# Performance work log

Measured on AMD Instinct MI355X. Metric: run time of the kernel, lower is better.

## Reference

```python
import jax, jax.numpy as jnp
import numpy as np

NUM_CLASSES = 81
NMS_THRESHOLD = 0.4
MAX_BOXES = 300
NEG = -1e9  # score used to mark suppressed / background boxes


def setup_inputs() -> dict:
    key = jax.random.key(0)
    k1, k2, k3, k4, k5 = jax.random.split(key, 5)
    N = 300000
    # realistic boxes: centers in [0,800), sizes in [1,101)
    cx = jax.random.uniform(k1, (N,), jnp.float32) * 800.0
    cy = jax.random.uniform(k2, (N,), jnp.float32) * 800.0
    w = jax.random.uniform(k3, (N,), jnp.float32) * 100.0 + 1.0
    h = jax.random.uniform(k4, (N,), jnp.float32) * 100.0 + 1.0
    boxes = jnp.stack([cx - w / 2, cy - h / 2, cx + w / 2, cy + h / 2], axis=-1)
    boxes = boxes[None]  # [1, N, 4]
    classification = jax.random.normal(k5, (1, N, NUM_CLASSES), jnp.float32)
    return {"boxes": boxes, "classification": classification}


def _nms_select(boxes, scores, max_boxes, iou_threshold):
    # boxes: [N,4] (x1,y1,x2,y2); scores: [N]. Greedy NMS, fixed max_boxes iterations.
    x1, y1, x2, y2 = boxes[:, 0], boxes[:, 1], boxes[:, 2], boxes[:, 3]
    areas = jnp.maximum(x2 - x1, 0.0) * jnp.maximum(y2 - y1, 0.0)

    def body(scores_c, _):
        idx = jnp.argmax(scores_c)
        valid = scores_c[idx] > NEG / 2
        b = boxes[idx]
        xx1 = jnp.maximum(b[0], x1)
        yy1 = jnp.maximum(b[1], y1)
        xx2 = jnp.minimum(b[2], x2)
        yy2 = jnp.minimum(b[3], y2)
        inter = jnp.maximum(xx2 - xx1, 0.0) * jnp.maximum(yy2 - yy1, 0.0)
        union = areas[idx] + areas - inter
        iou = inter / jnp.maximum(union, 1e-8)
        # suppress everything overlapping the selected box (includes itself, iou=1)
        new_scores = jnp.where(iou > iou_threshold, NEG, scores_c)
        return new_scores, (idx, valid)

    _, (idxs, valids) = jax.lax.scan(body, scores, None, length=max_boxes)
    return idxs, valids


def reference(boxes, classification):
    b = boxes.reshape(-1, 4)                      # [N,4]
    cls = classification.reshape(-1, NUM_CLASSES)  # [N,C]
    scores = jnp.max(cls, axis=1)                  # [N]
    labels = jnp.argmax(cls, axis=1)               # [N]
    # filter background (label==0) by masking scores instead of dynamic gather
    scores = jnp.where(labels > 0, scores, NEG)
    idxs, valid = _nms_select(b, scores, MAX_BOXES, NMS_THRESHOLD)
    v = valid[:, None].astype(b.dtype)
    out_boxes = b[idxs] * v                        # [max_boxes,4], zero-padded
    out_cls = cls[idxs] * v                        # [max_boxes,C], zero-padded
    return out_boxes[None], out_cls[None]
```

## Files before the change

kernel.cpp:

```cpp
#include <hip/hip_runtime.h>
#include <stdint.h>

#define NUM_CLASSES 81
#define MAX_BOXES 300
#define NEG_SCORE (-1000000000.0f)
#define IOU_THR 0.4f
#define MMAX 2048
#define MWORDS (MMAX / 64)

static constexpr size_t OFF_SCORES = 0;
static constexpr size_t OFF_CAREA  = 0x1F0000;
static constexpr size_t OFF_COARSE = 0x200000;
static constexpr size_t OFF_FINE   = 0x201000;
static constexpr size_t OFF_CTRL   = 0x202000;
static constexpr size_t OFF_RANK   = 0x203000;
static constexpr size_t OFF_KEYS   = 0x208000;
static constexpr size_t OFF_CIDX   = 0x210000;
static constexpr size_t OFF_CBOX   = 0x214000;
static constexpr size_t OFF_ACC    = 0x224000;
static constexpr size_t OFF_MATRIX = 0x228000;

__device__ __forceinline__ uint32_t float_ordered(float f) {
    uint32_t b = __float_as_uint(f);
    return (b & 0x80000000u) ? ~b : (b | 0x80000000u);
}

__device__ __forceinline__ uint64_t readlane_u64(uint64_t v, int srclane) {
    uint32_t lo = (uint32_t)__builtin_amdgcn_readlane((int)(uint32_t)v, srclane);
    uint32_t hi = (uint32_t)__builtin_amdgcn_readlane((int)(uint32_t)(v >> 32), srclane);
    return ((uint64_t)hi << 32) | lo;
}

__global__ void score_kernel(const float* __restrict__ cls, float* __restrict__ scores,
                             uint32_t* __restrict__ coarse, uint32_t* __restrict__ fine,
                             uint32_t* __restrict__ ctrl, uint32_t* __restrict__ rank, int n) {
    if (blockIdx.x == 0) {
        int t = threadIdx.x;
        if (t < 256) { coarse[t] = 0; fine[t] = 0; }
        if (t < 8) ctrl[t] = 0;
        for (int r = t; r < MMAX; r += 256) rank[r] = 0;
    }
    const int q = threadIdx.x & 15;
    const int box = blockIdx.x * 16 + (threadIdx.x >> 4);
    const int cbox = box < n ? box : n - 1;
    const float* row = cls + (size_t)cbox * NUM_CLASSES;

    float v[5];
    #pragma unroll
    for (int it = 0; it < 5; ++it) v[it] = row[it * 16 + q];
    float e80 = row[80];

    float m = v[0];
    #pragma unroll
    for (int it = 1; it < 5; ++it) m = fmaxf(m, v[it]);
    m = (q == 15) ? fmaxf(m, e80) : m;
    m = fmaxf(m, __shfl_xor(m, 1));
    m = fmaxf(m, __shfl_xor(m, 2));
    m = fmaxf(m, __shfl_xor(m, 4));
    m = fmaxf(m, __shfl_xor(m, 8));

    if (q == 0 && box < n) {
        scores[box] = (v[0] == m) ? NEG_SCORE : m;
    }
}

__global__ void coarse_hist_kernel(const float* __restrict__ scores, uint32_t* __restrict__ coarse, int n) {
    __shared__ uint32_t h[256];
    for (int t = threadIdx.x; t < 256; t += blockDim.x) h[t] = 0;
    __syncthreads();
    for (int i = blockIdx.x * blockDim.x + threadIdx.x; i < n; i += gridDim.x * blockDim.x) {
        uint32_t o = float_ordered(scores[i]);
        atomicAdd(&h[o >> 24], 1u);
    }
    __syncthreads();
    for (int t = threadIdx.x; t < 256; t += blockDim.x)
        if (h[t]) atomicAdd(&coarse[t], h[t]);
}

__device__ __forceinline__ int select_coarse(const uint32_t* coarse, uint32_t* above_out) {
    uint32_t s = 0;
    for (int c = 255; c >= 0; --c) {
        uint32_t sc = s + coarse[c];
        if (sc > MMAX) { *above_out = s; return c; }
        s = sc;
    }
    *above_out = s;
    return -1;
}

__global__ void fine_hist_kernel(const float* __restrict__ scores, const uint32_t* __restrict__ coarse,
                                 uint32_t* __restrict__ fine, int n) {
    __shared__ int sC;
    __shared__ uint32_t h[256];
    if (threadIdx.x == 0) {
        uint32_t above;
        sC = select_coarse(coarse, &above);
    }
    for (int t = threadIdx.x; t < 256; t += blockDim.x) h[t] = 0;
    __syncthreads();
    int C = sC;
    if (C < 0) return;
    for (int i = blockIdx.x * blockDim.x + threadIdx.x; i < n; i += gridDim.x * blockDim.x) {
        uint32_t o = float_ordered(scores[i]);
        if ((int)(o >> 24) == C) atomicAdd(&h[(o >> 16) & 255u], 1u);
    }
    __syncthreads();
    for (int t = threadIdx.x; t < 256; t += blockDim.x)
        if (h[t]) atomicAdd(&fine[t], h[t]);
}

__global__ void compact_kernel(const float* __restrict__ scores, const uint32_t* __restrict__ coarse,
                               const uint32_t* __restrict__ fine, uint32_t* __restrict__ ctrl,
                               uint64_t* __restrict__ keys, int n) {
    __shared__ uint32_t sThr;
    if (threadIdx.x == 0) {
        uint32_t above;
        int C = select_coarse(coarse, &above);
        uint32_t thr;
        if (C < 0) {
            thr = 0;
        } else {
            uint32_t R = MMAX - above;
            uint32_t g = 0, F = 0;
            for (int f = 255; f >= 0; --f) {
                uint32_t gf = g + fine[f];
                if (gf > R) { F = (uint32_t)f + 1u; break; }
                g = gf;
            }
            thr = ((uint32_t)C << 8) | F;
        }
        sThr = thr;
    }
    __syncthreads();
    uint32_t thr = sThr;
    for (int i = blockIdx.x * blockDim.x + threadIdx.x; i < n; i += gridDim.x * blockDim.x) {
        uint32_t o = float_ordered(scores[i]);
        if ((o >> 16) >= thr) {
            uint32_t pos = atomicAdd(&ctrl[0], 1u);
            if (pos < MMAX)
                keys[pos] = ((uint64_t)o << 32) | (uint32_t)(~(uint32_t)i);
        }
    }
}

__global__ void rank_partial_kernel(const uint64_t* __restrict__ keys, const uint32_t* __restrict__ ctrl,
                                    uint32_t* __restrict__ rank) {
    __shared__ uint64_t kk[256];
    int M = (int)ctrl[0]; if (M > MMAX) M = MMAX;
    int cbase = blockIdx.x * 256;
    int jbase = blockIdx.y * 256;
    if (cbase >= M || jbase >= M) return;
    int t = threadIdx.x;
    int j = jbase + t;
    kk[t] = (j < M) ? keys[j] : 0ull;
    __syncthreads();
    int c = cbase + t;
    if (c >= M) return;
    uint64_t k = keys[c];
    int cnt = 0;
    #pragma unroll 8
    for (int u = 0; u < 256; ++u) cnt += (kk[u] > k) ? 1 : 0;
    if (cnt) atomicAdd(&rank[c], (uint32_t)cnt);
}

__global__ void scatter_kernel(const uint64_t* __restrict__ keys, const uint32_t* __restrict__ rank,
                               const uint32_t* __restrict__ ctrl, const float* __restrict__ boxes,
                               int* __restrict__ csorted_idx, float4* __restrict__ csorted_box,
                               float* __restrict__ careas) {
    int M = (int)ctrl[0]; if (M > MMAX) M = MMAX;
    int c = blockIdx.x * blockDim.x + threadIdx.x;
    if (c >= M) return;
    uint64_t k = keys[c];
    uint32_t r = rank[c];
    uint32_t idx = ~(uint32_t)k;
    float4 b = *(const float4*)(boxes + (size_t)idx * 4);
    csorted_idx[r] = (int)idx;
    csorted_box[r] = b;
    careas[r] = fmaxf(b.z - b.x, 0.f) * fmaxf(b.w - b.y, 0.f);
}

__global__ void matrix_kernel(const float4* __restrict__ cbox, const float* __restrict__ careas,
                              const uint32_t* __restrict__ ctrl, uint64_t* __restrict__ matrix) {
    int i = blockIdx.x;
    int M = (int)ctrl[0]; if (M > MMAX) M = MMAX;
    if (i >= M) return;
    int lane = threadIdx.x & 63;
    int wave = threadIdx.x >> 6;
    float4 bi = cbox[i];
    float ai = careas[i];
    int w0 = i >> 6;
    for (int w = w0 + wave; w < MWORDS; w += 4) {
        int j = (w << 6) | lane;
        bool sup = false;
        if (j < M) {
            float4 bj = cbox[j];
            float xx1 = fmaxf(bi.x, bj.x);
            float yy1 = fmaxf(bi.y, bj.y);
            float xx2 = fminf(bi.z, bj.z);
            float yy2 = fminf(bi.w, bj.w);
            float inter = fmaxf(xx2 - xx1, 0.f) * fmaxf(yy2 - yy1, 0.f);
            float uni = ai + careas[j] - inter;
            float iou = inter / fmaxf(uni, 1e-8f);
            sup = iou > IOU_THR;
        }
        uint64_t word = __ballot(sup ? 1 : 0);
        if (lane == 0) matrix[(size_t)i * MWORDS + w] = word;
    }
}

typedef const uint32_t __attribute__((address_space(1)))* glb_u32p;
typedef uint32_t __attribute__((address_space(3)))* lds_u32p;

__global__ void scan_kernel(const uint64_t* __restrict__ matrix, uint32_t* __restrict__ ctrl,
                            int* __restrict__ accepted) {
    __shared__ uint64_t sbuf[2][64][MWORDS];
    const int lane = threadIdx.x;
    const int l31 = lane & 31;
    int M = (int)ctrl[0]; if (M > MMAX) M = MMAX;
    uint64_t removed = 0;
    uint64_t wrd = 0;
    int acc = 0;

#define STAGE(BI, BASE)                                                          \
    {                                                                            \
        _Pragma("unroll")                                                        \
        for (int r_ = 0; r_ < 64; ++r_) {                                        \
            const uint32_t* gsrc =                                               \
                (const uint32_t*)(matrix + (size_t)((BASE) + r_) * MWORDS) + lane; \
            __builtin_amdgcn_global_load_lds((glb_u32p)gsrc,                     \
                                             (lds_u32p)&sbuf[BI][r_][0], 4, 0, 0); \
        }                                                                        \
    }

#define PROCESS(BI, BASE)                                                        \
    {                                                                            \
        uint64_t W[16];                                                          \
        _Pragma("unroll")                                                        \
        for (int w_ = 0; w_ < 16; ++w_) W[w_] = sbuf[BI][w_][l31];               \
        _Pragma("unroll")                                                        \
        for (int r_ = 0; r_ < 64; ++r_) {                                        \
            int i_ = (BASE) + r_;                                                \
            uint64_t row = W[r_ & 15];                                           \
            if (r_ + 16 < 64) W[r_ & 15] = sbuf[BI][r_ + 16][l31];               \
            if (r_ == 0) wrd = readlane_u64(removed, i_ >> 6);                   \
            if (i_ < M && acc < MAX_BOXES && !((wrd >> (i_ & 63)) & 1ull)) {     \
                if (lane == 0) accepted[acc] = i_;                               \
                removed |= row;                                                  \
                wrd = readlane_u64(removed, i_ >> 6);                            \
                ++acc;                                                           \
            }                                                                    \
        }                                                                        \
    }

    int nblocks = (M + 63) >> 6;
    if (nblocks > 0) {
        STAGE(0, 0);
        asm volatile("s_waitcnt vmcnt(0)" ::: "memory");
        int bi = 0;
        for (int b = 0; b < nblocks && acc < MAX_BOXES; ++b) {
            if (b + 1 < nblocks) STAGE(bi ^ 1, (b + 1) << 6);
            PROCESS(bi, b << 6);
            asm volatile("s_waitcnt vmcnt(0)" ::: "memory");
            bi ^= 1;
        }
    }
#undef STAGE
#undef PROCESS
    if (lane == 0) ctrl[1] = (uint32_t)acc;
}

__global__ void output_kernel(const float* __restrict__ boxes, const float* __restrict__ cls,
                              const int* __restrict__ csorted_idx, const int* __restrict__ accepted,
                              const uint32_t* __restrict__ ctrl, float* __restrict__ out, int total) {
    int e = blockIdx.x * blockDim.x + threadIdx.x;
    if (e >= total) return;
    int acc = (int)ctrl[1];
    float val = 0.0f;
    if (e < MAX_BOXES * 4) {
        int s = e >> 2, f = e & 3;
        if (s < acc) {
            int orig = csorted_idx[accepted[s]];
            val = boxes[(size_t)orig * 4 + f];
        }
    } else {
        int e2 = e - MAX_BOXES * 4;
        int s = e2 / NUM_CLASSES;
        int c = e2 - s * NUM_CLASSES;
        if (s < acc) {
            int orig = csorted_idx[accepted[s]];
            val = cls[(size_t)orig * NUM_CLASSES + c];
        }
    }
    out[e] = val;
}

extern "C" void kernel_launch(void* const* d_in, const int* in_sizes, int n_in,
                              void* d_out, int out_size, void* d_ws, size_t ws_size,
                              hipStream_t stream) {
    const float* boxes = (const float*)d_in[0];
    const float* cls   = (const float*)d_in[1];
    float* out = (float*)d_out;
    const int N = in_sizes[0] / 4;

    char* ws = (char*)d_ws;
    float*     scores      = (float*)(ws + OFF_SCORES);
    float*     careas      = (float*)(ws + OFF_CAREA);
    uint32_t*  coarse      = (uint32_t*)(ws + OFF_COARSE);
    uint32_t*  fine        = (uint32_t*)(ws + OFF_FINE);
    uint32_t*  ctrl        = (uint32_t*)(ws + OFF_CTRL);
    uint32_t*  rank        = (uint32_t*)(ws + OFF_RANK);
    uint64_t*  keys        = (uint64_t*)(ws + OFF_KEYS);
    int*       csorted_idx = (int*)(ws + OFF_CIDX);
    float4*    csorted_box = (float4*)(ws + OFF_CBOX);
    int*       accepted    = (int*)(ws + OFF_ACC);
    uint64_t*  matrix      = (uint64_t*)(ws + OFF_MATRIX);

    score_kernel<<<(N + 15) / 16, 256, 0, stream>>>(cls, scores, coarse, fine, ctrl, rank, N);
    coarse_hist_kernel<<<256, 256, 0, stream>>>(scores, coarse, N);
    fine_hist_kernel<<<256, 256, 0, stream>>>(scores, coarse, fine, N);
    compact_kernel<<<512, 256, 0, stream>>>(scores, coarse, fine, ctrl, keys, N);
    rank_partial_kernel<<<dim3(MMAX / 256, MMAX / 256), 256, 0, stream>>>(keys, ctrl, rank);
    scatter_kernel<<<MMAX / 256, 256, 0, stream>>>(keys, rank, ctrl, boxes, csorted_idx,
                                                   csorted_box, careas);
    matrix_kernel<<<MMAX, 256, 0, stream>>>(csorted_box, careas, ctrl, matrix);
    scan_kernel<<<1, 64, 0, stream>>>(matrix, ctrl, accepted);
    output_kernel<<<(out_size + 255) / 256, 256, 0, stream>>>(boxes, cls, csorted_idx, accepted,
                                                              ctrl, out, out_size);
}
```

Before: 109.0 us.

## Fuse all NMS stages into one cooperative persistent kernel with grid syncs

Replaces the nine separate kernel launches with a single cooperative kernel of 256 blocks that runs every stage in turn, separated by grid.sync(). The rank and scatter steps are merged: each of 8 blocks loads all keys into LDS and computes full ranks directly, so the rank buffer and its atomics go away. The aim is to remove per-launch overhead and inter-kernel gaps. In exchange, grid-wide barriers are paid at every stage, occupancy is limited to 256 blocks (the score pass over 300k rows now loops), and the large shared-memory union may reduce how many blocks fit per CU.

```diff
diff --git a/kernel.cpp b/kernel.cpp
--- a/kernel.cpp
+++ b/kernel.cpp
@@ -1,5 +1,8 @@
 #include <hip/hip_runtime.h>
+#include <hip/hip_cooperative_groups.h>
 #include <stdint.h>
+
+namespace cg = cooperative_groups;
 
 #define NUM_CLASSES 81
 #define MAX_BOXES 300
@@ -7,13 +10,14 @@
 #define IOU_THR 0.4f
 #define MMAX 2048
 #define MWORDS (MMAX / 64)
+#define GRID_BLOCKS 256
+#define BLOCK_THREADS 256
 
 static constexpr size_t OFF_SCORES = 0;
 static constexpr size_t OFF_CAREA  = 0x1F0000;
 static constexpr size_t OFF_COARSE = 0x200000;
 static constexpr size_t OFF_FINE   = 0x201000;
 static constexpr size_t OFF_CTRL   = 0x202000;
-static constexpr size_t OFF_RANK   = 0x203000;
 static constexpr size_t OFF_KEYS   = 0x208000;
 static constexpr size_t OFF_CIDX   = 0x210000;
 static constexpr size_t OFF_CBOX   = 0x214000;
@@ -29,52 +33,6 @@
     uint32_t lo = (uint32_t)__builtin_amdgcn_readlane((int)(uint32_t)v, srclane);
     uint32_t hi = (uint32_t)__builtin_amdgcn_readlane((int)(uint32_t)(v >> 32), srclane);
     return ((uint64_t)hi << 32) | lo;
-}
-
-__global__ void score_kernel(const float* __restrict__ cls, float* __restrict__ scores,
-                             uint32_t* __restrict__ coarse, uint32_t* __restrict__ fine,
-                             uint32_t* __restrict__ ctrl, uint32_t* __restrict__ rank, int n) {
-    if (blockIdx.x == 0) {
-        int t = threadIdx.x;
-        if (t < 256) { coarse[t] = 0; fine[t] = 0; }
-        if (t < 8) ctrl[t] = 0;
-        for (int r = t; r < MMAX; r += 256) rank[r] = 0;
-    }
-    const int q = threadIdx.x & 15;
-    const int box = blockIdx.x * 16 + (threadIdx.x >> 4);
-    const int cbox = box < n ? box : n - 1;
-    const float* row = cls + (size_t)cbox * NUM_CLASSES;
-
-    float v[5];
-    #pragma unroll
-    for (int it = 0; it < 5; ++it) v[it] = row[it * 16 + q];
-    float e80 = row[80];
-
-    float m = v[0];
-    #pragma unroll
-    for (int it = 1; it < 5; ++it) m = fmaxf(m, v[it]);
-    m = (q == 15) ? fmaxf(m, e80) : m;
-    m = fmaxf(m, __shfl_xor(m, 1));
-    m = fmaxf(m, __shfl_xor(m, 2));
-    m = fmaxf(m, __shfl_xor(m, 4));
-    m = fmaxf(m, __shfl_xor(m, 8));
-
-    if (q == 0 && box < n) {
-        scores[box] = (v[0] == m) ? NEG_SCORE : m;
-    }
-}
-
-__global__ void coarse_hist_kernel(const float* __restrict__ scores, uint32_t* __restrict__ coarse, int n) {
-    __shared__ uint32_t h[256];
-    for (int t = threadIdx.x; t < 256; t += blockDim.x) h[t] = 0;
-    __syncthreads();
-    for (int i = blockIdx.x * blockDim.x + threadIdx.x; i < n; i += gridDim.x * blockDim.x) {
-        uint32_t o = float_ordered(scores[i]);
-        atomicAdd(&h[o >> 24], 1u);
-    }
-    __syncthreads();
-    for (int t = threadIdx.x; t < 256; t += blockDim.x)
-        if (h[t]) atomicAdd(&coarse[t], h[t]);
 }
 
 __device__ __forceinline__ int select_coarse(const uint32_t* coarse, uint32_t* above_out) {
@@ -88,32 +46,95 @@
     return -1;
 }
 
-__global__ void fine_hist_kernel(const float* __restrict__ scores, const uint32_t* __restrict__ coarse,
-                                 uint32_t* __restrict__ fine, int n) {
+typedef const uint32_t __attribute__((address_space(1)))* glb_u32p;
+typedef uint32_t __attribute__((address_space(3)))* lds_u32p;
+
+union SmemU {
+    uint32_t h[256];
+    uint64_t kk[MMAX];
+    uint64_t sbuf[2][64][MWORDS];
+};
+
+__global__ void __launch_bounds__(BLOCK_THREADS) nms_mega(
+    const float* __restrict__ boxes, const float* __restrict__ cls,
+    float* __restrict__ out, char* __restrict__ ws, int n, int out_total) {
+    cg::grid_group grid = cg::this_grid();
+
+    float*     scores      = (float*)(ws + OFF_SCORES);
+    float*     careas      = (float*)(ws + OFF_CAREA);
+    uint32_t*  coarse      = (uint32_t*)(ws + OFF_COARSE);
+    uint32_t*  fine        = (uint32_t*)(ws + OFF_FINE);
+    uint32_t*  ctrl        = (uint32_t*)(ws + OFF_CTRL);
+    uint64_t*  keys        = (uint64_t*)(ws + OFF_KEYS);
+    int*       csorted_idx = (int*)(ws + OFF_CIDX);
+    float4*    csorted_box = (float4*)(ws + OFF_CBOX);
+    int*       accepted    = (int*)(ws + OFF_ACC);
+    uint64_t*  matrix      = (uint64_t*)(ws + OFF_MATRIX);
+
+    __shared__ SmemU sm;
     __shared__ int sC;
-    __shared__ uint32_t h[256];
-    if (threadIdx.x == 0) {
-        uint32_t above;
-        sC = select_coarse(coarse, &above);
-    }
-    for (int t = threadIdx.x; t < 256; t += blockDim.x) h[t] = 0;
-    __syncthreads();
-    int C = sC;
-    if (C < 0) return;
-    for (int i = blockIdx.x * blockDim.x + threadIdx.x; i < n; i += gridDim.x * blockDim.x) {
-        uint32_t o = float_ordered(scores[i]);
-        if ((int)(o >> 24) == C) atomicAdd(&h[(o >> 16) & 255u], 1u);
-    }
-    __syncthreads();
-    for (int t = threadIdx.x; t < 256; t += blockDim.x)
-        if (h[t]) atomicAdd(&fine[t], h[t]);
-}
-
-__global__ void compact_kernel(const float* __restrict__ scores, const uint32_t* __restrict__ coarse,
-                               const uint32_t* __restrict__ fine, uint32_t* __restrict__ ctrl,
-                               uint64_t* __restrict__ keys, int n) {
     __shared__ uint32_t sThr;
-    if (threadIdx.x == 0) {
+
+    const int tid = threadIdx.x;
+    const int bid = blockIdx.x;
+    const int nb  = gridDim.x;
+
+    if (bid == 0) {
+        if (tid < 256) { coarse[tid] = 0; fine[tid] = 0; }
+        if (tid < 8) ctrl[tid] = 0;
+    }
+    {
+        const int q = tid & 15;
+        const int g = tid >> 4;
+        for (int b0 = bid * 16; b0 < n; b0 += nb * 16) {
+            int box = b0 + g;
+            int cbox = box < n ? box : n - 1;
+            const float* row = cls + (size_t)cbox * NUM_CLASSES;
+            float v[5];
+            #pragma unroll
+            for (int it = 0; it < 5; ++it) v[it] = row[it * 16 + q];
+            float e80 = row[80];
+            float m = v[0];
+            #pragma unroll
+            for (int it = 1; it < 5; ++it) m = fmaxf(m, v[it]);
+            m = (q == 15) ? fmaxf(m, e80) : m;
+            m = fmaxf(m, __shfl_xor(m, 1));
+            m = fmaxf(m, __shfl_xor(m, 2));
+            m = fmaxf(m, __shfl_xor(m, 4));
+            m = fmaxf(m, __shfl_xor(m, 8));
+            if (q == 0 && box < n)
+                scores[box] = (v[0] == m) ? NEG_SCORE : m;
+        }
+    }
+    grid.sync();
+
+    for (int t = tid; t < 256; t += BLOCK_THREADS) sm.h[t] = 0;
+    __syncthreads();
+    for (int i = bid * BLOCK_THREADS + tid; i < n; i += nb * BLOCK_THREADS)
+        atomicAdd(&sm.h[float_ordered(scores[i]) >> 24], 1u);
+    __syncthreads();
+    for (int t = tid; t < 256; t += BLOCK_THREADS)
+        if (sm.h[t]) atomicAdd(&coarse[t], sm.h[t]);
+    grid.sync();
+
+    if (tid == 0) { uint32_t ab; sC = select_coarse(coarse, &ab); }
+    for (int t = tid; t < 256; t += BLOCK_THREADS) sm.h[t] = 0;
+    __syncthreads();
+    {
+        int C = sC;
+        if (C >= 0) {
+            for (int i = bid * BLOCK_THREADS + tid; i < n; i += nb * BLOCK_THREADS) {
+                uint32_t o = float_ordered(scores[i]);
+                if ((int)(o >> 24) == C) atomicAdd(&sm.h[(o >> 16) & 255u], 1u);
+            }
+        }
+    }
+    __syncthreads();
+    for (int t = tid; t < 256; t += BLOCK_THREADS)
+        if (sm.h[t]) atomicAdd(&fine[t], sm.h[t]);
+    grid.sync();
+
+    if (tid == 0) {
         uint32_t above;
         int C = select_coarse(coarse, &above);
         uint32_t thr;
@@ -132,166 +153,147 @@
         sThr = thr;
     }
     __syncthreads();
-    uint32_t thr = sThr;
-    for (int i = blockIdx.x * blockDim.x + threadIdx.x; i < n; i += gridDim.x * blockDim.x) {
-        uint32_t o = float_ordered(scores[i]);
-        if ((o >> 16) >= thr) {
-            uint32_t pos = atomicAdd(&ctrl[0], 1u);
-            if (pos < MMAX)
-                keys[pos] = ((uint64_t)o << 32) | (uint32_t)(~(uint32_t)i);
-        }
-    }
-}
-
-__global__ void rank_partial_kernel(const uint64_t* __restrict__ keys, const uint32_t* __restrict__ ctrl,
-                                    uint32_t* __restrict__ rank) {
-    __shared__ uint64_t kk[256];
+    {
+        uint32_t thr = sThr;
+        for (int i = bid * BLOCK_THREADS + tid; i < n; i += nb * BLOCK_THREADS) {
+            uint32_t o = float_ordered(scores[i]);
+            if ((o >> 16) >= thr) {
+                uint32_t pos = atomicAdd(&ctrl[0], 1u);
+                if (pos < MMAX)
+                    keys[pos] = ((uint64_t)o << 32) | (uint32_t)(~(uint32_t)i);
+            }
+        }
+    }
+    grid.sync();
+
     int M = (int)ctrl[0]; if (M > MMAX) M = MMAX;
-    int cbase = blockIdx.x * 256;
-    int jbase = blockIdx.y * 256;
-    if (cbase >= M || jbase >= M) return;
-    int t = threadIdx.x;
-    int j = jbase + t;
-    kk[t] = (j < M) ? keys[j] : 0ull;
-    __syncthreads();
-    int c = cbase + t;
-    if (c >= M) return;
-    uint64_t k = keys[c];
-    int cnt = 0;
-    #pragma unroll 8
-    for (int u = 0; u < 256; ++u) cnt += (kk[u] > k) ? 1 : 0;
-    if (cnt) atomicAdd(&rank[c], (uint32_t)cnt);
-}
-
-__global__ void scatter_kernel(const uint64_t* __restrict__ keys, const uint32_t* __restrict__ rank,
-                               const uint32_t* __restrict__ ctrl, const float* __restrict__ boxes,
-                               int* __restrict__ csorted_idx, float4* __restrict__ csorted_box,
-                               float* __restrict__ careas) {
-    int M = (int)ctrl[0]; if (M > MMAX) M = MMAX;
-    int c = blockIdx.x * blockDim.x + threadIdx.x;
-    if (c >= M) return;
-    uint64_t k = keys[c];
-    uint32_t r = rank[c];
-    uint32_t idx = ~(uint32_t)k;
-    float4 b = *(const float4*)(boxes + (size_t)idx * 4);
-    csorted_idx[r] = (int)idx;
-    csorted_box[r] = b;
-    careas[r] = fmaxf(b.z - b.x, 0.f) * fmaxf(b.w - b.y, 0.f);
-}
-
-__global__ void matrix_kernel(const float4* __restrict__ cbox, const float* __restrict__ careas,
-                              const uint32_t* __restrict__ ctrl, uint64_t* __restrict__ matrix) {
-    int i = blockIdx.x;
-    int M = (int)ctrl[0]; if (M > MMAX) M = MMAX;
-    if (i >= M) return;
-    int lane = threadIdx.x & 63;
-    int wave = threadIdx.x >> 6;
-    float4 bi = cbox[i];
-    float ai = careas[i];
-    int w0 = i >> 6;
-    for (int w = w0 + wave; w < MWORDS; w += 4) {
-        int j = (w << 6) | lane;
-        bool sup = false;
-        if (j < M) {
-            float4 bj = cbox[j];
-            float xx1 = fmaxf(bi.x, bj.x);
-            float yy1 = fmaxf(bi.y, bj.y);
-            float xx2 = fminf(bi.z, bj.z);
-            float yy2 = fminf(bi.w, bj.w);
-            float inter = fmaxf(xx2 - xx1, 0.f) * fmaxf(yy2 - yy1, 0.f);
-            float uni = ai + careas[j] - inter;
-            float iou = inter / fmaxf(uni, 1e-8f);
-            sup = iou > IOU_THR;
-        }
-        uint64_t word = __ballot(sup ? 1 : 0);
-        if (lane == 0) matrix[(size_t)i * MWORDS + w] = word;
-    }
-}
-
-typedef const uint32_t __attribute__((address_space(1)))* glb_u32p;
-typedef uint32_t __attribute__((address_space(3)))* lds_u32p;
-
-__global__ void scan_kernel(const uint64_t* __restrict__ matrix, uint32_t* __restrict__ ctrl,
-                            int* __restrict__ accepted) {
-    __shared__ uint64_t sbuf[2][64][MWORDS];
-    const int lane = threadIdx.x;
-    const int l31 = lane & 31;
-    int M = (int)ctrl[0]; if (M > MMAX) M = MMAX;
-    uint64_t removed = 0;
-    uint64_t wrd = 0;
-    int acc = 0;
-
-#define STAGE(BI, BASE)                                                          \
-    {                                                                            \
-        _Pragma("unroll")                                                        \
-        for (int r_ = 0; r_ < 64; ++r_) {                                        \
-            const uint32_t* gsrc =                                               \
+
+    if (bid < MMAX / BLOCK_THREADS) {
+        for (int i = tid; i < MMAX; i += BLOCK_THREADS)
+            sm.kk[i] = (i < M) ? keys[i] : 0ull;
+        __syncthreads();
+        int c = bid * BLOCK_THREADS + tid;
+        if (c < M) {
+            uint64_t k = sm.kk[c];
+            int cnt = 0;
+            #pragma unroll 8
+            for (int u = 0; u < MMAX; ++u) cnt += (sm.kk[u] > k) ? 1 : 0;
+            uint32_t idx = ~(uint32_t)k;
+            float4 b = *(const float4*)(boxes + (size_t)idx * 4);
+            csorted_idx[cnt] = (int)idx;
+            csorted_box[cnt] = b;
+            careas[cnt] = fmaxf(b.z - b.x, 0.f) * fmaxf(b.w - b.y, 0.f);
+        }
+        __syncthreads();
+    }
+    grid.sync();
+
+    {
+        int lane = tid & 63;
+        int wave = tid >> 6;
+        for (int i = bid; i < M; i += nb) {
+            float4 bi = csorted_box[i];
+            float ai = careas[i];
+            int w0 = i >> 6;
+            for (int w = w0 + wave; w < MWORDS; w += 4) {
+                int j = (w << 6) | lane;
+                bool sup = false;
+                if (j < M) {
+                    float4 bj = csorted_box[j];
+                    float xx1 = fmaxf(bi.x, bj.x);
+                    float yy1 = fmaxf(bi.y, bj.y);
+                    float xx2 = fminf(bi.z, bj.z);
+                    float yy2 = fminf(bi.w, bj.w);
+                    float inter = fmaxf(xx2 - xx1, 0.f) * fmaxf(yy2 - yy1, 0.f);
+                    float uni = ai + careas[j] - inter;
+                    float iou = inter / fmaxf(uni, 1e-8f);
+                    sup = iou > IOU_THR;
+                }
+                uint64_t word = __ballot(sup ? 1 : 0);
+                if (lane == 0) matrix[(size_t)i * MWORDS + w] = word;
+            }
+        }
+    }
+    grid.sync();
+
+    if (bid == 0 && tid < 64) {
+        const int lane = tid;
+        const int l31 = lane & 31;
+        uint64_t removed = 0;
+        uint64_t wrd = 0;
+        int acc = 0;
+
+#define STAGE(BI, BASE)                                                            \
+    {                                                                              \
+        _Pragma("unroll")                                                          \
+        for (int r_ = 0; r_ < 64; ++r_) {                                          \
+            const uint32_t* gsrc =                                                 \
                 (const uint32_t*)(matrix + (size_t)((BASE) + r_) * MWORDS) + lane; \
-            __builtin_amdgcn_global_load_lds((glb_u32p)gsrc,                     \
-                                             (lds_u32p)&sbuf[BI][r_][0], 4, 0, 0); \
-        }                                                                        \
-    }
-
-#define PROCESS(BI, BASE)                                                        \
-    {                                                                            \
-        uint64_t W[16];                                                          \
-        _Pragma("unroll")                                                        \
-        for (int w_ = 0; w_ < 16; ++w_) W[w_] = sbuf[BI][w_][l31];               \
-        _Pragma("unroll")                                                        \
-        for (int r_ = 0; r_ < 64; ++r_) {                                        \
-            int i_ = (BASE) + r_;                                                \
-            uint64_t row = W[r_ & 15];                                           \
-            if (r_ + 16 < 64) W[r_ & 15] = sbuf[BI][r_ + 16][l31];               \
-            if (r_ == 0) wrd = readlane_u64(removed, i_ >> 6);                   \
-            if (i_ < M && acc < MAX_BOXES && !((wrd >> (i_ & 63)) & 1ull)) {     \
-                if (lane == 0) accepted[acc] = i_;                               \
-                removed |= row;                                                  \
-                wrd = readlane_u64(removed, i_ >> 6);                            \
-                ++acc;                                                           \
-            }                                                                    \
-        }                                                                        \
-    }
-
-    int nblocks = (M + 63) >> 6;
-    if (nblocks > 0) {
-        STAGE(0, 0);
-        asm volatile("s_waitcnt vmcnt(0)" ::: "memory");
-        int bi = 0;
-        for (int b = 0; b < nblocks && acc < MAX_BOXES; ++b) {
-            if (b + 1 < nblocks) STAGE(bi ^ 1, (b + 1) << 6);
-            PROCESS(bi, b << 6);
+            __builtin_amdgcn_global_load_lds((glb_u32p)gsrc,                       \
+                                             (lds_u32p)&sm.sbuf[BI][r_][0], 4, 0, 0); \
+        }                                                                          \
+    }
+
+#define PROCESS(BI, BASE)                                                          \
+    {                                                                              \
+        uint64_t W[16];                                                            \
+        _Pragma("unroll")                                                          \
+        for (int w_ = 0; w_ < 16; ++w_) W[w_] = sm.sbuf[BI][w_][l31];              \
+        _Pragma("unroll")                                                          \
+        for (int r_ = 0; r_ < 64; ++r_) {                                          \
+            int i_ = (BASE) + r_;                                                  \
+            uint64_t row = W[r_ & 15];                                             \
+            if (r_ + 16 < 64) W[r_ & 15] = sm.sbuf[BI][r_ + 16][l31];              \
+            if (r_ == 0) wrd = readlane_u64(removed, i_ >> 6);                     \
+            if (i_ < M && acc < MAX_BOXES && !((wrd >> (i_ & 63)) & 1ull)) {       \
+                if (lane == 0) accepted[acc] = i_;                                 \
+                removed |= row;                                                    \
+                wrd = readlane_u64(removed, i_ >> 6);                              \
+                ++acc;                                                             \
+            }                                                                      \
+        }                                                                          \
+    }
+
+        int nblocks = (M + 63) >> 6;
+        if (nblocks > 0) {
+            STAGE(0, 0);
             asm volatile("s_waitcnt vmcnt(0)" ::: "memory");
-            bi ^= 1;
-        }
-    }
+            int bi = 0;
+            for (int b = 0; b < nblocks && acc < MAX_BOXES; ++b) {
+                if (b + 1 < nblocks) STAGE(bi ^ 1, (b + 1) << 6);
+                PROCESS(bi, b << 6);
+                asm volatile("s_waitcnt vmcnt(0)" ::: "memory");
+                bi ^= 1;
+            }
+        }
 #undef STAGE
 #undef PROCESS
-    if (lane == 0) ctrl[1] = (uint32_t)acc;
-}
-
-__global__ void output_kernel(const float* __restrict__ boxes, const float* __restrict__ cls,
-                              const int* __restrict__ csorted_idx, const int* __restrict__ accepted,
-                              const uint32_t* __restrict__ ctrl, float* __restrict__ out, int total) {
-    int e = blockIdx.x * blockDim.x + threadIdx.x;
-    if (e >= total) return;
-    int acc = (int)ctrl[1];
-    float val = 0.0f;
-    if (e < MAX_BOXES * 4) {
-        int s = e >> 2, f = e & 3;
-        if (s < acc) {
-            int orig = csorted_idx[accepted[s]];
-            val = boxes[(size_t)orig * 4 + f];
-        }
-    } else {
-        int e2 = e - MAX_BOXES * 4;
-        int s = e2 / NUM_CLASSES;
-        int c = e2 - s * NUM_CLASSES;
-        if (s < acc) {
-            int orig = csorted_idx[accepted[s]];
-            val = cls[(size_t)orig * NUM_CLASSES + c];
-        }
-    }
-    out[e] = val;
+        if (lane == 0) ctrl[1] = (uint32_t)acc;
+    }
+    grid.sync();
+
+    {
+        int acc = (int)ctrl[1];
+        for (int e = bid * BLOCK_THREADS + tid; e < out_total; e += nb * BLOCK_THREADS) {
+            float val = 0.0f;
+            if (e < MAX_BOXES * 4) {
+                int s = e >> 2, f = e & 3;
+                if (s < acc) {
+                    int orig = csorted_idx[accepted[s]];
+                    val = boxes[(size_t)orig * 4 + f];
+                }
+            } else {
+                int e2 = e - MAX_BOXES * 4;
+                int s = e2 / NUM_CLASSES;
+                int c = e2 - s * NUM_CLASSES;
+                if (s < acc) {
+                    int orig = csorted_idx[accepted[s]];
+                    val = cls[(size_t)orig * NUM_CLASSES + c];
+                }
+            }
+            out[e] = val;
+        }
+    }
 }
 
 extern "C" void kernel_launch(void* const* d_in, const int* in_sizes, int n_in,
@@ -300,30 +302,12 @@
     const float* boxes = (const float*)d_in[0];
     const float* cls   = (const float*)d_in[1];
     float* out = (float*)d_out;
-    const int N = in_sizes[0] / 4;
-
     char* ws = (char*)d_ws;
-    float*     scores      = (float*)(ws + OFF_SCORES);
-    float*     careas      = (float*)(ws + OFF_CAREA);
-    uint32_t*  coarse      = (uint32_t*)(ws + OFF_COARSE);
-    uint32_t*  fine        = (uint32_t*)(ws + OFF_FINE);
-    uint32_t*  ctrl        = (uint32_t*)(ws + OFF_CTRL);
-    uint32_t*  rank        = (uint32_t*)(ws + OFF_RANK);
-    uint64_t*  keys        = (uint64_t*)(ws + OFF_KEYS);
-    int*       csorted_idx = (int*)(ws + OFF_CIDX);
-    float4*    csorted_box = (float4*)(ws + OFF_CBOX);
-    int*       accepted    = (int*)(ws + OFF_ACC);
-    uint64_t*  matrix      = (uint64_t*)(ws + OFF_MATRIX);
-
-    score_kernel<<<(N + 15) / 16, 256, 0, stream>>>(cls, scores, coarse, fine, ctrl, rank, N);
-    coarse_hist_kernel<<<256, 256, 0, stream>>>(scores, coarse, N);
-    fine_hist_kernel<<<256, 256, 0, stream>>>(scores, coarse, fine, N);
-    compact_kernel<<<512, 256, 0, stream>>>(scores, coarse, fine, ctrl, keys, N);
-    rank_partial_kernel<<<dim3(MMAX / 256, MMAX / 256), 256, 0, stream>>>(keys, ctrl, rank);
-    scatter_kernel<<<MMAX / 256, 256, 0, stream>>>(keys, rank, ctrl, boxes, csorted_idx,
-                                                   csorted_box, careas);
-    matrix_kernel<<<MMAX, 256, 0, stream>>>(csorted_box, careas, ctrl, matrix);
-    scan_kernel<<<1, 64, 0, stream>>>(matrix, ctrl, accepted);
-    output_kernel<<<(out_size + 255) / 256, 256, 0, stream>>>(boxes, cls, csorted_idx, accepted,
-                                                              ctrl, out, out_size);
-}
+    int N = in_sizes[0] / 4;
+    int out_total = out_size;
+
+    void* args[] = {(void*)&boxes, (void*)&cls, (void*)&out, (void*)&ws,
+                    (void*)&N, (void*)&out_total};
+    hipLaunchCooperativeKernel((const void*)nms_mega, dim3(GRID_BLOCKS),
+                               dim3(BLOCK_THREADS), args, 0, stream);
+}
```

Measured after the change: 345.2 us. +216.5%, slower.

## Fuse rank+scatter and scan+output kernels, widen score kernel per-thread work

Applied to the files above, without the earlier changes.

Merges the partial-rank and scatter kernels into one kernel, where each block loads all candidate keys into LDS and computes full ranks without atomics. It also fuses the NMS scan with output gathering in a single 1024-thread block, keeping accepted indices in LDS. Together these remove two launches and the rank/accepted global buffers. The score kernel now uses 8 threads per box instead of 16. The cost is a serial O(M) rank loop per thread, and output writes done by a single block instead of a full grid.

```diff
diff --git a/kernel.cpp b/kernel.cpp
--- a/kernel.cpp
+++ b/kernel.cpp
@@ -13,11 +13,9 @@
 static constexpr size_t OFF_COARSE = 0x200000;
 static constexpr size_t OFF_FINE   = 0x201000;
 static constexpr size_t OFF_CTRL   = 0x202000;
-static constexpr size_t OFF_RANK   = 0x203000;
 static constexpr size_t OFF_KEYS   = 0x208000;
 static constexpr size_t OFF_CIDX   = 0x210000;
 static constexpr size_t OFF_CBOX   = 0x214000;
-static constexpr size_t OFF_ACC    = 0x224000;
 static constexpr size_t OFF_MATRIX = 0x228000;
 
 __device__ __forceinline__ uint32_t float_ordered(float f) {
@@ -33,33 +31,31 @@
 
 __global__ void score_kernel(const float* __restrict__ cls, float* __restrict__ scores,
                              uint32_t* __restrict__ coarse, uint32_t* __restrict__ fine,
-                             uint32_t* __restrict__ ctrl, uint32_t* __restrict__ rank, int n) {
+                             uint32_t* __restrict__ ctrl, int n) {
     if (blockIdx.x == 0) {
         int t = threadIdx.x;
         if (t < 256) { coarse[t] = 0; fine[t] = 0; }
         if (t < 8) ctrl[t] = 0;
-        for (int r = t; r < MMAX; r += 256) rank[r] = 0;
-    }
-    const int q = threadIdx.x & 15;
-    const int box = blockIdx.x * 16 + (threadIdx.x >> 4);
+    }
+    const int r = threadIdx.x & 7;
+    const int box = blockIdx.x * 32 + (threadIdx.x >> 3);
     const int cbox = box < n ? box : n - 1;
     const float* row = cls + (size_t)cbox * NUM_CLASSES;
 
-    float v[5];
+    float v[10];
     #pragma unroll
-    for (int it = 0; it < 5; ++it) v[it] = row[it * 16 + q];
+    for (int it = 0; it < 10; ++it) v[it] = row[it * 8 + r];
     float e80 = row[80];
 
     float m = v[0];
     #pragma unroll
-    for (int it = 1; it < 5; ++it) m = fmaxf(m, v[it]);
-    m = (q == 15) ? fmaxf(m, e80) : m;
+    for (int it = 1; it < 10; ++it) m = fmaxf(m, v[it]);
+    m = fmaxf(m, e80);
     m = fmaxf(m, __shfl_xor(m, 1));
     m = fmaxf(m, __shfl_xor(m, 2));
     m = fmaxf(m, __shfl_xor(m, 4));
-    m = fmaxf(m, __shfl_xor(m, 8));
-
-    if (q == 0 && box < n) {
+
+    if (r == 0 && box < n) {
         scores[box] = (v[0] == m) ? NEG_SCORE : m;
     }
 }
@@ -143,40 +139,27 @@
     }
 }
 
-__global__ void rank_partial_kernel(const uint64_t* __restrict__ keys, const uint32_t* __restrict__ ctrl,
-                                    uint32_t* __restrict__ rank) {
-    __shared__ uint64_t kk[256];
+__global__ void rank_scatter_kernel(const uint64_t* __restrict__ keys, const uint32_t* __restrict__ ctrl,
+                                    const float* __restrict__ boxes,
+                                    int* __restrict__ csorted_idx, float4* __restrict__ csorted_box,
+                                    float* __restrict__ careas) {
+    __shared__ uint64_t kk[MMAX];
     int M = (int)ctrl[0]; if (M > MMAX) M = MMAX;
-    int cbase = blockIdx.x * 256;
-    int jbase = blockIdx.y * 256;
-    if (cbase >= M || jbase >= M) return;
     int t = threadIdx.x;
-    int j = jbase + t;
-    kk[t] = (j < M) ? keys[j] : 0ull;
-    __syncthreads();
-    int c = cbase + t;
+    for (int i = t; i < MMAX; i += blockDim.x)
+        kk[i] = (i < M) ? keys[i] : 0ull;
+    __syncthreads();
+    int c = blockIdx.x * blockDim.x + t;
     if (c >= M) return;
-    uint64_t k = keys[c];
+    uint64_t k = kk[c];
     int cnt = 0;
     #pragma unroll 8
-    for (int u = 0; u < 256; ++u) cnt += (kk[u] > k) ? 1 : 0;
-    if (cnt) atomicAdd(&rank[c], (uint32_t)cnt);
-}
-
-__global__ void scatter_kernel(const uint64_t* __restrict__ keys, const uint32_t* __restrict__ rank,
-                               const uint32_t* __restrict__ ctrl, const float* __restrict__ boxes,
-                               int* __restrict__ csorted_idx, float4* __restrict__ csorted_box,
-                               float* __restrict__ careas) {
-    int M = (int)ctrl[0]; if (M > MMAX) M = MMAX;
-    int c = blockIdx.x * blockDim.x + threadIdx.x;
-    if (c >= M) return;
-    uint64_t k = keys[c];
-    uint32_t r = rank[c];
+    for (int u = 0; u < MMAX; ++u) cnt += (kk[u] > k) ? 1 : 0;
     uint32_t idx = ~(uint32_t)k;
     float4 b = *(const float4*)(boxes + (size_t)idx * 4);
-    csorted_idx[r] = (int)idx;
-    csorted_box[r] = b;
-    careas[r] = fmaxf(b.z - b.x, 0.f) * fmaxf(b.w - b.y, 0.f);
+    csorted_idx[cnt] = (int)idx;
+    csorted_box[cnt] = b;
+    careas[cnt] = fmaxf(b.z - b.x, 0.f) * fmaxf(b.w - b.y, 0.f);
 }
 
 __global__ void matrix_kernel(const float4* __restrict__ cbox, const float* __restrict__ careas,
@@ -211,87 +194,91 @@
 typedef const uint32_t __attribute__((address_space(1)))* glb_u32p;
 typedef uint32_t __attribute__((address_space(3)))* lds_u32p;
 
-__global__ void scan_kernel(const uint64_t* __restrict__ matrix, uint32_t* __restrict__ ctrl,
-                            int* __restrict__ accepted) {
+__global__ void __launch_bounds__(1024) scan_output_kernel(
+    const uint64_t* __restrict__ matrix, const uint32_t* __restrict__ ctrl,
+    const float* __restrict__ boxes, const float* __restrict__ cls,
+    const int* __restrict__ csorted_idx, float* __restrict__ out, int out_total) {
     __shared__ uint64_t sbuf[2][64][MWORDS];
-    const int lane = threadIdx.x;
-    const int l31 = lane & 31;
+    __shared__ int s_accepted[MAX_BOXES];
+    __shared__ int s_acc;
     int M = (int)ctrl[0]; if (M > MMAX) M = MMAX;
-    uint64_t removed = 0;
-    uint64_t wrd = 0;
-    int acc = 0;
-
-#define STAGE(BI, BASE)                                                          \
-    {                                                                            \
-        _Pragma("unroll")                                                        \
-        for (int r_ = 0; r_ < 64; ++r_) {                                        \
-            const uint32_t* gsrc =                                               \
+
+    if (threadIdx.x < 64) {
+        const int lane = threadIdx.x;
+        const int l31 = lane & 31;
+        uint64_t removed = 0;
+        uint64_t wrd = 0;
+        int acc = 0;
+
+#define STAGE(BI, BASE)                                                            \
+    {                                                                              \
+        _Pragma("unroll")                                                          \
+        for (int r_ = 0; r_ < 64; ++r_) {                                          \
+            const uint32_t* gsrc =                                                 \
                 (const uint32_t*)(matrix + (size_t)((BASE) + r_) * MWORDS) + lane; \
-            __builtin_amdgcn_global_load_lds((glb_u32p)gsrc,                     \
+            __builtin_amdgcn_global_load_lds((glb_u32p)gsrc,                       \
                                              (lds_u32p)&sbuf[BI][r_][0], 4, 0, 0); \
-        }                                                                        \
-    }
-
-#define PROCESS(BI, BASE)                                                        \
-    {                                                                            \
-        uint64_t W[16];                                                          \
-        _Pragma("unroll")                                                        \
-        for (int w_ = 0; w_ < 16; ++w_) W[w_] = sbuf[BI][w_][l31];               \
-        _Pragma("unroll")                                                        \
-        for (int r_ = 0; r_ < 64; ++r_) {                                        \
-            int i_ = (BASE) + r_;                                                \
-            uint64_t row = W[r_ & 15];                                           \
-            if (r_ + 16 < 64) W[r_ & 15] = sbuf[BI][r_ + 16][l31];               \
-            if (r_ == 0) wrd = readlane_u64(removed, i_ >> 6);                   \
-            if (i_ < M && acc < MAX_BOXES && !((wrd >> (i_ & 63)) & 1ull)) {     \
-                if (lane == 0) accepted[acc] = i_;                               \
-                removed |= row;                                                  \
-                wrd = readlane_u64(removed, i_ >> 6);                            \
-                ++acc;                                                           \
-            }                                                                    \
-        }                                                                        \
-    }
-
-    int nblocks = (M + 63) >> 6;
-    if (nblocks > 0) {
-        STAGE(0, 0);
-        asm volatile("s_waitcnt vmcnt(0)" ::: "memory");
-        int bi = 0;
-        for (int b = 0; b < nblocks && acc < MAX_BOXES; ++b) {
-            if (b + 1 < nblocks) STAGE(bi ^ 1, (b + 1) << 6);
-            PROCESS(bi, b << 6);
+        }                                                                          \
+    }
+
+#define PROCESS(BI, BASE)                                                          \
+    {                                                                              \
+        uint64_t W[16];                                                            \
+        _Pragma("unroll")                                                          \
+        for (int w_ = 0; w_ < 16; ++w_) W[w_] = sbuf[BI][w_][l31];                 \
+        _Pragma("unroll")                                                          \
+        for (int r_ = 0; r_ < 64; ++r_) {                                          \
+            int i_ = (BASE) + r_;                                                  \
+            uint64_t row = W[r_ & 15];                                             \
+            if (r_ + 16 < 64) W[r_ & 15] = sbuf[BI][r_ + 16][l31];                 \
+            if (r_ == 0) wrd = readlane_u64(removed, i_ >> 6);                     \
+            if (i_ < M && acc < MAX_BOXES && !((wrd >> (i_ & 63)) & 1ull)) {       \
+                if (lane == 0) s_accepted[acc] = i_;                               \
+                removed |= row;                                                    \
+                wrd = readlane_u64(removed, i_ >> 6);                              \
+                ++acc;                                                             \
+            }                                                                      \
+        }                                                                          \
+    }
+
+        int nblocks = (M + 63) >> 6;
+        if (nblocks > 0) {
+            STAGE(0, 0);
             asm volatile("s_waitcnt vmcnt(0)" ::: "memory");
-            bi ^= 1;
-        }
-    }
+            int bi = 0;
+            for (int b = 0; b < nblocks && acc < MAX_BOXES; ++b) {
+                if (b + 1 < nblocks) STAGE(bi ^ 1, (b + 1) << 6);
+                PROCESS(bi, b << 6);
+                asm volatile("s_waitcnt vmcnt(0)" ::: "memory");
+                bi ^= 1;
+            }
+        }
 #undef STAGE
 #undef PROCESS
-    if (lane == 0) ctrl[1] = (uint32_t)acc;
-}
-
-__global__ void output_kernel(const float* __restrict__ boxes, const float* __restrict__ cls,
-                              const int* __restrict__ csorted_idx, const int* __restrict__ accepted,
-                              const uint32_t* __restrict__ ctrl, float* __restrict__ out, int total) {
-    int e = blockIdx.x * blockDim.x + threadIdx.x;
-    if (e >= total) return;
-    int acc = (int)ctrl[1];
-    float val = 0.0f;
-    if (e < MAX_BOXES * 4) {
-        int s = e >> 2, f = e & 3;
-        if (s < acc) {
-            int orig = csorted_idx[accepted[s]];
-            val = boxes[(size_t)orig * 4 + f];
-        }
-    } else {
-        int e2 = e - MAX_BOXES * 4;
-        int s = e2 / NUM_CLASSES;
-        int c = e2 - s * NUM_CLASSES;
-        if (s < acc) {
-            int orig = csorted_idx[accepted[s]];
-            val = cls[(size_t)orig * NUM_CLASSES + c];
-        }
-    }
-    out[e] = val;
+        if (lane == 0) s_acc = acc;
+    }
+    __syncthreads();
+
+    int acc = s_acc;
+    for (int e = threadIdx.x; e < out_total; e += 1024) {
+        float val = 0.0f;
+        if (e < MAX_BOXES * 4) {
+            int s = e >> 2, f = e & 3;
+            if (s < acc) {
+                int orig = csorted_idx[s_accepted[s]];
+                val = boxes[(size_t)orig * 4 + f];
+            }
+        } else {
+            int e2 = e - MAX_BOXES * 4;
+            int s = e2 / NUM_CLASSES;
+            int c = e2 - s * NUM_CLASSES;
+            if (s < acc) {
+                int orig = csorted_idx[s_accepted[s]];
+                val = cls[(size_t)orig * NUM_CLASSES + c];
+            }
+        }
+        out[e] = val;
+    }
 }
 
 extern "C" void kernel_launch(void* const* d_in, const int* in_sizes, int n_in,
@@ -308,22 +295,18 @@
     uint32_t*  coarse      = (uint32_t*)(ws + OFF_COARSE);
     uint32_t*  fine        = (uint32_t*)(ws + OFF_FINE);
     uint32_t*  ctrl        = (uint32_t*)(ws + OFF_CTRL);
-    uint32_t*  rank        = (uint32_t*)(ws + OFF_RANK);
     uint64_t*  keys        = (uint64_t*)(ws + OFF_KEYS);
     int*       csorted_idx = (int*)(ws + OFF_CIDX);
     float4*    csorted_box = (float4*)(ws + OFF_CBOX);
-    int*       accepted    = (int*)(ws + OFF_ACC);
     uint64_t*  matrix      = (uint64_t*)(ws + OFF_MATRIX);
 
-    score_kernel<<<(N + 15) / 16, 256, 0, stream>>>(cls, scores, coarse, fine, ctrl, rank, N);
+    score_kernel<<<(N + 31) / 32, 256, 0, stream>>>(cls, scores, coarse, fine, ctrl, N);
     coarse_hist_kernel<<<256, 256, 0, stream>>>(scores, coarse, N);
     fine_hist_kernel<<<256, 256, 0, stream>>>(scores, coarse, fine, N);
     compact_kernel<<<512, 256, 0, stream>>>(scores, coarse, fine, ctrl, keys, N);
-    rank_partial_kernel<<<dim3(MMAX / 256, MMAX / 256), 256, 0, stream>>>(keys, ctrl, rank);
-    scatter_kernel<<<MMAX / 256, 256, 0, stream>>>(keys, rank, ctrl, boxes, csorted_idx,
-                                                   csorted_box, careas);
+    rank_scatter_kernel<<<MMAX / 256, 256, 0, stream>>>(keys, ctrl, boxes, csorted_idx,
+                                                        csorted_box, careas);
     matrix_kernel<<<MMAX, 256, 0, stream>>>(csorted_box, careas, ctrl, matrix);
-    scan_kernel<<<1, 64, 0, stream>>>(matrix, ctrl, accepted);
-    output_kernel<<<(out_size + 255) / 256, 256, 0, stream>>>(boxes, cls, csorted_idx, accepted,
-                                                              ctrl, out, out_size);
-}
+    scan_output_kernel<<<1, 1024, 0, stream>>>(matrix, ctrl, boxes, cls, csorted_idx,
+                                               out, out_size);
+}
```

Result: slower. 143.7 us (+31.8%).
